# Optimization experiments

Hardware: AMD Instinct MI355X
Metric: run time of the kernel (lower is better)

The kernel has to match this reference:

```python
import jax, jax.numpy as jnp
import numpy as np
from jax import lax

B = 32768   # batch_size
M = 14      # letters per word
H, WD = 16, 8  # input_dim -> cout_numel = 128 (SAME padding, stride 1)
L = 26      # num_labels
KS = 5      # conv kernel size (conv_layers[0][-1])
F = H * WD


def setup_inputs() -> dict:
    key = jax.random.key(0)
    k1, k2, k3, k4, k5 = jax.random.split(key, 5)
    X = jax.random.normal(k1, (B, M, F), dtype=jnp.float32)
    K = jax.random.normal(k2, (1, 1, KS, KS), dtype=jnp.float32) * 0.1  # conv kernel (OIHW)
    b = jax.random.normal(k3, (1,), dtype=jnp.float32) * 0.1            # conv bias
    W = jax.random.normal(k4, (L, F), dtype=jnp.float32)                # emission weights
    T = jax.random.normal(k5, (L, L), dtype=jnp.float32)                # transition matrix
    return {"X": X, "K": K, "b": b, "W": W, "T": T}


def _conv_features(X, K, b):
    # each letter image is a (1,H,W) map; SAME conv keeps spatial dims -> F features
    words = X.reshape(B * M, 1, H, WD)
    out = lax.conv_general_dilated(
        words, K, window_strides=(1, 1), padding="SAME",
        dimension_numbers=("NCHW", "OIHW", "NCHW")) + b
    return out.reshape(B, M, F)


def _viterbi(score, T):
    # score: (M, L) emission scores for one word; Viterbi max-decode
    def step(v, s):  # v: (L,) best path value ending at each label
        tot = v[:, None] + T          # (prev L, next L)
        bp = jnp.argmax(tot, axis=0)  # best previous label per next label
        v_new = jnp.max(tot, axis=0) + s
        return v_new, bp

    v_last, bps = lax.scan(step, score[0], score[1:])  # bps: (M-1, L)
    last = jnp.argmax(v_last)

    def back(nxt, bp):
        cur = bp[nxt]
        return cur, cur

    _, idxs = lax.scan(back, last, bps, reverse=True)  # (M-1,)
    path = jnp.concatenate([idxs, last[None]])         # (M,)
    return path.astype(jnp.int32)


def reference(X, K, b, W, T):
    feats = _conv_features(X, K, b)                 # (B, M, F)
    scores = jnp.einsum("bmf,lf->bml", feats, W)    # (B, M, L) emission scores
    decods = jax.vmap(lambda s: _viterbi(s, T))(scores)  # (B, M)
    return decods[..., None]                        # (B, M, 1) int32, matches torch output
```

## Files before the change

### kernel.cpp

```cpp
#include <hip/hip_runtime.h>
#include <math.h>

#define LBL 26
#define MM  14
#define FF  128
#define HH  16
#define WW  8
#define KSZ 5
#define WPB 16
#define LPB (WPB * MM)
#define SST 29

__global__ void prep_kernel(const float* __restrict__ K,
                            const float* __restrict__ b,
                            const float* __restrict__ W,
                            float* __restrict__ w2,
                            float* __restrict__ cvec) {
    int idx = blockIdx.x * blockDim.x + threadIdx.x;
    int stride = gridDim.x * blockDim.x;
    for (int o = idx; o < LBL * FF; o += stride) {
        int l = o / FF, f = o % FF;
        int qy = f / WW, qx = f % WW;
        double acc = 0.0;
        for (int ky = 0; ky < KSZ; ++ky) {
            int y = qy - ky + 2;
            if (y < 0 || y >= HH) continue;
            for (int kx = 0; kx < KSZ; ++kx) {
                int x = qx - kx + 2;
                if (x < 0 || x >= WW) continue;
                acc += (double)K[ky * KSZ + kx] * (double)W[l * FF + y * WW + x];
            }
        }
        w2[o] = (float)acc;
    }
    for (int l = idx; l < LBL; l += stride) {
        double s = 0.0;
        for (int f = 0; f < FF; ++f) s += (double)W[l * FF + f];
        cvec[l] = (float)(s * (double)b[0]);
    }
}

__global__ __launch_bounds__(256) void fused_kernel(const float* __restrict__ X,
                                                    const float* __restrict__ w2,
                                                    const float* __restrict__ cvec,
                                                    const float* __restrict__ Tm,
                                                    int* __restrict__ out) {
    __shared__ float4 wtile[32][LBL];
    __shared__ float  s_lds[WPB][MM][SST];
    __shared__ float  vb[8][32];

    const int tid = threadIdx.x;
    const int blk = blockIdx.x;

    const float4* W4 = (const float4*)w2;
    for (int i = tid; i < 32 * LBL; i += 256) {
        const int l = i >> 5, q = i & 31;
        wtile[q][l] = W4[i];
    }
    __syncthreads();

    if (tid < LPB) {
        const int letter = blk * LPB + tid;
        const float4* xr = (const float4*)X + (size_t)letter * 32;

        float acc[LBL];
#pragma unroll
        for (int l = 0; l < LBL; ++l) acc[l] = cvec[l];

#define COMPUTE(g, C0, C1, C2, C3)                                         \
    {                                                                      \
        _Pragma("unroll")                                                  \
        for (int l = 0; l < LBL; ++l) {                                    \
            const float4 w0 = wtile[4 * (g) + 0][l];        \
            const float4 w1 = wtile[4 * (g) + 1][l];                       \
            const float4 w2v = wtile[4 * (g) + 2][l];                      \
            const float4 w3 = wtile[4 * (g) + 3][l];                       \
            float a = acc[l];                                              \
            a = fmaf(C0.x, w0.x, a); a = fmaf(C0.y, w0.y, a);              \
            a = fmaf(C0.z, w0.z, a); a = fmaf(C0.w, w0.w, a);              \
            a = fmaf(C1.x, w1.x, a); a = fmaf(C1.y, w1.y, a);              \
            a = fmaf(C1.z, w1.z, a); a = fmaf(C1.w, w1.w, a);              \
            a = fmaf(C2.x, w2v.x, a); a = fmaf(C2.y, w2v.y, a);            \
            a = fmaf(C2.z, w2v.z, a); a = fmaf(C2.w, w2v.w, a);            \
            a = fmaf(C3.x, w3.x, a); a = fmaf(C3.y, w3.y, a);              \
            a = fmaf(C3.z, w3.z, a); a = fmaf(C3.w, w3.w, a);              \
            acc[l] = a;                                                    \
        }                                                                  \
    }

        float4 c0 = xr[0], c1 = xr[1], c2 = xr[2], c3 = xr[3];
        for (int g = 0; g < 7; ++g) {
            const float4 n0 = xr[4 * g + 4], n1 = xr[4 * g + 5];
            const float4 n2 = xr[4 * g + 6], n3 = xr[4 * g + 7];
            COMPUTE(g, c0, c1, c2, c3)
            c0 = n0; c1 = n1; c2 = n2; c3 = n3;
        }
        COMPUTE(7, c0, c1, c2, c3)
#undef COMPUTE

        float* dst = &s_lds[0][0][0] + tid * SST;
#pragma unroll
        for (int l = 0; l < LBL; ++l) dst[l] = acc[l];
    }
    __syncthreads();

    const int wv   = tid >> 6;
    const int lane = tid & 63;
    const int half = lane >> 5;
    const int j    = lane & 31;
    const int jc   = (j < LBL) ? j : 25;

    const int wl = wv * 2 + half;

    float tcol[LBL];
#pragma unroll
    for (int i = 0; i < LBL; ++i) tcol[i] = Tm[i * LBL + jc];

    float* vbw = &vb[wl][0];

    for (int pass = 0; pass < 2; ++pass) {
        const int lwl  = pass * 8 + wl;
        const int word = blk * WPB + lwl;
        const float* sw = &s_lds[lwl][0][0];

        float v = (j < LBL) ? sw[j] : -INFINITY;
        vbw[j] = v;
        unsigned bp_pack[4] = {0u, 0u, 0u, 0u};

#pragma unroll
        for (int t = 1; t < MM; ++t) {
            const float se = sw[t * SST + jc];
            float best = -INFINITY;
            int bi = 0;
            const float4* q4 = (const float4*)vbw;
#define VCHK(vexpr, idx) { const float val = (vexpr) + tcol[idx]; \
                           if (val > best) { best = val; bi = idx; } }
            {
                float4 qq;
                qq = q4[0]; VCHK(qq.x, 0) VCHK(qq.y, 1) VCHK(qq.z, 2) VCHK(qq.w, 3)
                qq = q4[1]; VCHK(qq.x, 4) VCHK(qq.y, 5) VCHK(qq.z, 6) VCHK(qq.w, 7)
                qq = q4[2]; VCHK(qq.x, 8) VCHK(qq.y, 9) VCHK(qq.z, 10) VCHK(qq.w, 11)
                qq = q4[3]; VCHK(qq.x, 12) VCHK(qq.y, 13) VCHK(qq.z, 14) VCHK(qq.w, 15)
                qq = q4[4]; VCHK(qq.x, 16) VCHK(qq.y, 17) VCHK(qq.z, 18) VCHK(qq.w, 19)
                qq = q4[5]; VCHK(qq.x, 20) VCHK(qq.y, 21) VCHK(qq.z, 22) VCHK(qq.w, 23)
                qq = q4[6]; VCHK(qq.x, 24) VCHK(qq.y, 25)
            }
#undef VCHK
            v = (j < LBL) ? (best + se) : -INFINITY;
            vbw[j] = v;
            const int k = t - 1;
            bp_pack[k >> 2] |= (unsigned)bi << ((k & 3) * 8);
        }

        float best = v;
        int bidx = (j < LBL) ? j : 999;
#pragma unroll
        for (int d = 1; d < 32; d <<= 1) {
            const float ov = __shfl_xor(best, d, 64);
            const int oi = __shfl_xor(bidx, d, 64);
            if (ov > best || (ov == best && oi < bidx)) { best = ov; bidx = oi; }
        }

        int cur = bidx;
        if (j == 0) out[word * MM + (MM - 1)] = cur;
#pragma unroll
        for (int k = MM - 2; k >= 0; --k) {
            const unsigned packed = __shfl(bp_pack[k >> 2], (lane & 32) | cur, 64);
            cur = (int)((packed >> ((k & 3) * 8)) & 0xffu);
            if (j == 0) out[word * MM + k] = cur;
        }
    }
}

template <int PAD>
__global__ __launch_bounds__(256) void scores_kernel(const float* __restrict__ X,
                                                     const float* __restrict__ w2,
                                                     const float* __restrict__ cvec,
                                                     float* __restrict__ sV) {
    __shared__ float4 wtile[32][LBL];
    __shared__ float  slds[256 * LBL];

    const int tid    = threadIdx.x;
    const int letter = blockIdx.x * 256 + tid;

    const float4* W4 = (const float4*)w2;
    for (int i = tid; i < 32 * LBL; i += 256) {
        const int l = i >> 5, q = i & 31;
        wtile[q][l] = W4[i];
    }
    __syncthreads();

    const float4* xr = (const float4*)X + (size_t)letter * 32;

    float acc[LBL];
#pragma unroll
    for (int l = 0; l < LBL; ++l) acc[l] = cvec[l];

#define COMPUTE(g, C0, C1, C2, C3)                                         \
    {                                                                      \
        _Pragma("unroll")                                                  \
        for (int l = 0; l < LBL; ++l) {                                    \
            const float4 w0 = wtile[4 * (g) + 0][l];                       \
            const float4 w1 = wtile[4 * (g) + 1][l];                       \
            const float4 w2v = wtile[4 * (g) + 2][l];                      \
            const float4 w3 = wtile[4 * (g) + 3][l];                       \
            float a = acc[l];                                              \
            a = fmaf(C0.x, w0.x, a); a = fmaf(C0.y, w0.y, a);              \
            a = fmaf(C0.z, w0.z, a); a = fmaf(C0.w, w0.w, a);              \
            a = fmaf(C1.x, w1.x, a); a = fmaf(C1.y, w1.y, a);              \
            a = fmaf(C1.z, w1.z, a); a = fmaf(C1.w, w1.w, a);              \
            a = fmaf(C2.x, w2v.x, a); a = fmaf(C2.y, w2v.y, a);            \
            a = fmaf(C2.z, w2v.z, a); a = fmaf(C2.w, w2v.w, a);            \
            a = fmaf(C3.x, w3.x, a); a = fmaf(C3.y, w3.y, a);              \
            a = fmaf(C3.z, w3.z, a); a = fmaf(C3.w, w3.w, a);              \
            acc[l] = a;                                                    \
        }                                                                  \
    }

    float4 c0 = xr[0], c1 = xr[1], c2 = xr[2], c3 = xr[3];
    for (int g = 0; g < 7; ++g) {
        const float4 n0 = xr[4 * g + 4], n1 = xr[4 * g + 5];
        const float4 n2 = xr[4 * g + 6], n3 = xr[4 * g + 7];
        COMPUTE(g, c0, c1, c2, c3)
        c0 = n0; c1 = n1; c2 = n2; c3 = n3;
    }
    COMPUTE(7, c0, c1, c2, c3)
#undef COMPUTE

#pragma unroll
    for (int l = 0; l < LBL; ++l) slds[tid * LBL + l] = acc[l];
    __syncthreads();
    const size_t obase = (size_t)blockIdx.x * 256 * PAD;
    for (int idx = tid; idx < 256 * PAD; idx += 256) {
        const int ll = idx / PAD, lw = idx - ll * PAD;
        sV[obase + idx] = (lw < LBL) ? slds[ll * LBL + lw] : 0.0f;
    }
}

template <int PAD>
__global__ __launch_bounds__(256) void viterbi_kernel(const float* __restrict__ sV,
                                                      const float* __restrict__ Tm,
                                                      int* __restrict__ out) {
    __shared__ float T_lds[LBL * LBL];
    __shared__ float vb[8][32];

    const int tid  = threadIdx.x;
    for (int i = tid; i < LBL * LBL; i += 256) T_lds[i] = Tm[i];
    __syncthreads();

    const int wv   = tid >> 6;
    const int lane = tid & 63;
    const int half = lane >> 5;
    const int j    = lane & 31;
    const int jc   = (j < LBL) ? j : 25;

    const int wl   = wv * 2 + half;
    const int word = blockIdx.x * 8 + wl;
    const float* sw = sV + (size_t)word * (MM * PAD);

    float tcol[LBL];
#pragma unroll
    for (int i = 0; i < LBL; ++i) tcol[i] = T_lds[i * LBL + jc];

    float* vbw = &vb[wl][0];
    float v = (j < LBL) ? sw[j] : -INFINITY;
    vbw[j] = v;
    unsigned bp_pack[4] = {0u, 0u, 0u, 0u};

#pragma unroll
    for (int t = 1; t < MM; ++t) {
        const float se = sw[t * PAD + jc];
        float best = -INFINITY;
        int bi = 0;
        const float4* q4 = (const float4*)vbw;
#define VCHK(vexpr, idx) { const float val = (vexpr) + tcol[idx]; \
                           if (val > best) { best = val; bi = idx; } }
        {
            float4 qq;
            qq = q4[0]; VCHK(qq.x, 0) VCHK(qq.y, 1) VCHK(qq.z, 2) VCHK(qq.w, 3)
            qq = q4[1]; VCHK(qq.x, 4) VCHK(qq.y, 5) VCHK(qq.z, 6) VCHK(qq.w, 7)
            qq = q4[2]; VCHK(qq.x, 8) VCHK(qq.y, 9) VCHK(qq.z, 10) VCHK(qq.w, 11)
            qq = q4[3]; VCHK(qq.x, 12) VCHK(qq.y, 13) VCHK(qq.z, 14) VCHK(qq.w, 15)
            qq = q4[4]; VCHK(qq.x, 16) VCHK(qq.y, 17) VCHK(qq.z, 18) VCHK(qq.w, 19)
            qq = q4[5]; VCHK(qq.x, 20) VCHK(qq.y, 21) VCHK(qq.z, 22) VCHK(qq.w, 23)
            qq = q4[6]; VCHK(qq.x, 24) VCHK(qq.y, 25)
        }
#undef VCHK
        v = (j < LBL) ? (best + se) : -INFINITY;
        vbw[j] = v;
        const int k = t - 1;
        bp_pack[k >> 2] |= (unsigned)bi << ((k & 3) * 8);
    }

    float best = v;
    int bidx = (j < LBL) ? j : 999;
#pragma unroll
    for (int d = 1; d < 32; d <<= 1) {
        const float ov = __shfl_xor(best, d, 64);
        const int oi = __shfl_xor(bidx, d, 64);
        if (ov > best || (ov == best && oi < bidx)) { best = ov; bidx = oi; }
    }

    int cur = bidx;
    if (j == 0) out[word * MM + (MM - 1)] = cur;
#pragma unroll
    for (int k = MM - 2; k >= 0; --k) {
        const unsigned packed = __shfl(bp_pack[k >> 2], (lane & 32) | cur, 64);
        cur = (int)((packed >> ((k & 3) * 8)) & 0xffu);
        if (j == 0) out[word * MM + k] = cur;
    }
}

extern "C" void kernel_launch(void* const* d_in, const int* in_sizes, int n_in,
                              void* d_out, int out_size, void* d_ws, size_t ws_size,
                              hipStream_t stream) {
    const float* X = (const float*)d_in[0];
    const float* K = (const float*)d_in[1];
    const float* b = (const float*)d_in[2];
    const float* W = (const float*)d_in[3];
    const float* T = (const float*)d_in[4];
    int* out = (int*)d_out;

    const int nw = in_sizes[0] / (MM * FF);
    const int NLET = nw * MM;

    const size_t w_bytes = (size_t)(LBL * FF + LBL) * sizeof(float);
    const size_t sV28    = (size_t)NLET * 28 * sizeof(float);

    if ((NLET % LPB) == 0 && (nw % WPB) == 0 && ws_size >= w_bytes) {
        float* w2   = (float*)d_ws;
        float* cvec = w2 + LBL * FF;
        prep_kernel<<<(LBL * FF + 255) / 256, 256, 0, stream>>>(K, b, W, w2, cvec);
        fused_kernel<<<NLET / LPB, 256, 0, stream>>>(X, w2, cvec, T, out);
    } else if ((NLET % 256) == 0 && (nw % 8) == 0 && ws_size >= sV28 + w_bytes) {
        float* sV   = (float*)d_ws;
        float* w2   = (float*)((char*)d_ws + sV28);
        float* cvec = w2 + LBL * FF;
        prep_kernel<<<(LBL * FF + 255) / 256, 256, 0, stream>>>(K, b, W, w2, cvec);
        scores_kernel<28><<<NLET / 256, 256, 0, stream>>>(X, w2, cvec, sV);
        viterbi_kernel<28><<<nw / 8, 256, 0, stream>>>(sV, T, out);
    }
}
```

Before: 149.9 us.

## Fold conv-weight prep into scores kernel with packed FMA, drop fused kernel

Removes the fused single-kernel path and the separate prep kernel. The scores kernel now computes the conv-folded emission weights and bias vector in every block, in double precision, into an interleaved LDS layout. Its dot products use v_pk_fma_f32 over label pairs to halve FMA instruction count. The cost is redundant per-block weight preparation and a round trip of the score matrix through global memory into a separate Viterbi kernel, replacing the previous fused path.

```diff
diff --git a/kernel.cpp b/kernel.cpp
--- a/kernel.cpp
+++ b/kernel.cpp
@@ -7,9 +7,16 @@
 #define HH  16
 #define WW  8
 #define KSZ 5
-#define WPB 16
-#define LPB (WPB * MM)
-#define SST 29
+
+typedef float fv2 __attribute__((ext_vector_type(2)));
+
+__device__ __forceinline__ fv2 mkfv2(float a, float b) { fv2 r; r.x = a; r.y = b; return r; }
+
+__device__ __forceinline__ fv2 pkfma(fv2 a, fv2 b, fv2 c) {
+    fv2 d;
+    asm volatile("v_pk_fma_f32 %0, %1, %2, %3" : "=v"(d) : "v"(a), "v"(b), "v"(c));
+    return d;
+}
 
 __global__ void prep_kernel(const float* __restrict__ K,
                             const float* __restrict__ b,
@@ -40,143 +47,104 @@
     }
 }
 
-__global__ __launch_bounds__(256) void fused_kernel(const float* __restrict__ X,
-                                                    const float* __restrict__ w2,
-                                                    const float* __restrict__ cvec,
-                                                    const float* __restrict__ Tm,
-                                                    int* __restrict__ out) {
-    __shared__ float4 wtile[32][LBL];
-    __shared__ float  s_lds[WPB][MM][SST];
-    __shared__ float  vb[8][32];
-
-    const int tid = threadIdx.x;
-    const int blk = blockIdx.x;
-
-    const float4* W4 = (const float4*)w2;
-    for (int i = tid; i < 32 * LBL; i += 256) {
-        const int l = i >> 5, q = i & 31;
-        wtile[q][l] = W4[i];
-    }
-    __syncthreads();
-
-    if (tid < LPB) {
-        const int letter = blk * LPB + tid;
-        const float4* xr = (const float4*)X + (size_t)letter * 32;
-
-        float acc[LBL];
-#pragma unroll
-        for (int l = 0; l < LBL; ++l) acc[l] = cvec[l];
-
-#define COMPUTE(g, C0, C1, C2, C3)                                         \
-    {                                                                      \
-        _Pragma("unroll")                                                  \
-        for (int l = 0; l < LBL; ++l) {                                    \
-            const float4 w0 = wtile[4 * (g) + 0][l];        \
-            const float4 w1 = wtile[4 * (g) + 1][l];                       \
-            const float4 w2v = wtile[4 * (g) + 2][l];                      \
-            const float4 w3 = wtile[4 * (g) + 3][l];                       \
-            float a = acc[l];                                              \
-            a = fmaf(C0.x, w0.x, a); a = fmaf(C0.y, w0.y, a);              \
-            a = fmaf(C0.z, w0.z, a); a = fmaf(C0.w, w0.w, a);              \
-            a = fmaf(C1.x, w1.x, a); a = fmaf(C1.y, w1.y, a);              \
-            a = fmaf(C1.z, w1.z, a); a = fmaf(C1.w, w1.w, a);              \
-            a = fmaf(C2.x, w2v.x, a); a = fmaf(C2.y, w2v.y, a);            \
-            a = fmaf(C2.z, w2v.z, a); a = fmaf(C2.w, w2v.w, a);            \
-            a = fmaf(C3.x, w3.x, a); a = fmaf(C3.y, w3.y, a);              \
-            a = fmaf(C3.z, w3.z, a); a = fmaf(C3.w, w3.w, a);              \
-            acc[l] = a;                                                    \
-        }                                                                  \
-    }
-
-        float4 c0 = xr[0], c1 = xr[1], c2 = xr[2], c3 = xr[3];
-        for (int g = 0; g < 7; ++g) {
-            const float4 n0 = xr[4 * g + 4], n1 = xr[4 * g + 5];
-            const float4 n2 = xr[4 * g + 6], n3 = xr[4 * g + 7];
-            COMPUTE(g, c0, c1, c2, c3)
-            c0 = n0; c1 = n1; c2 = n2; c3 = n3;
-        }
-        COMPUTE(7, c0, c1, c2, c3)
-#undef COMPUTE
-
-        float* dst = &s_lds[0][0][0] + tid * SST;
-#pragma unroll
-        for (int l = 0; l < LBL; ++l) dst[l] = acc[l];
-    }
-    __syncthreads();
-
-    const int wv   = tid >> 6;
-    const int lane = tid & 63;
-    const int half = lane >> 5;
-    const int j    = lane & 31;
-    const int jc   = (j < LBL) ? j : 25;
-
-    const int wl = wv * 2 + half;
-
-    float tcol[LBL];
-#pragma unroll
-    for (int i = 0; i < LBL; ++i) tcol[i] = Tm[i * LBL + jc];
-
-    float* vbw = &vb[wl][0];
-
-    for (int pass = 0; pass < 2; ++pass) {
-        const int lwl  = pass * 8 + wl;
-        const int word = blk * WPB + lwl;
-        const float* sw = &s_lds[lwl][0][0];
-
-        float v = (j < LBL) ? sw[j] : -INFINITY;
-        vbw[j] = v;
-        unsigned bp_pack[4] = {0u, 0u, 0u, 0u};
-
-#pragma unroll
-        for (int t = 1; t < MM; ++t) {
-            const float se = sw[t * SST + jc];
-            float best = -INFINITY;
-            int bi = 0;
-            const float4* q4 = (const float4*)vbw;
-#define VCHK(vexpr, idx) { const float val = (vexpr) + tcol[idx]; \
-                           if (val > best) { best = val; bi = idx; } }
-            {
-                float4 qq;
-                qq = q4[0]; VCHK(qq.x, 0) VCHK(qq.y, 1) VCHK(qq.z, 2) VCHK(qq.w, 3)
-                qq = q4[1]; VCHK(qq.x, 4) VCHK(qq.y, 5) VCHK(qq.z, 6) VCHK(qq.w, 7)
-                qq = q4[2]; VCHK(qq.x, 8) VCHK(qq.y, 9) VCHK(qq.z, 10) VCHK(qq.w, 11)
-                qq = q4[3]; VCHK(qq.x, 12) VCHK(qq.y, 13) VCHK(qq.z, 14) VCHK(qq.w, 15)
-                qq = q4[4]; VCHK(qq.x, 16) VCHK(qq.y, 17) VCHK(qq.z, 18) VCHK(qq.w, 19)
-                qq = q4[5]; VCHK(qq.x, 20) VCHK(qq.y, 21) VCHK(qq.z, 22) VCHK(qq.w, 23)
-                qq = q4[6]; VCHK(qq.x, 24) VCHK(qq.y, 25)
-            }
-#undef VCHK
-            v = (j < LBL) ? (best + se) : -INFINITY;
-            vbw[j] = v;
-            const int k = t - 1;
-            bp_pack[k >> 2] |= (unsigned)bi << ((k & 3) * 8);
-        }
-
-        float best = v;
-        int bidx = (j < LBL) ? j : 999;
-#pragma unroll
-        for (int d = 1; d < 32; d <<= 1) {
-            const float ov = __shfl_xor(best, d, 64);
-            const int oi = __shfl_xor(bidx, d, 64);
-            if (ov > best || (ov == best && oi < bidx)) { best = ov; bidx = oi; }
-        }
-
-        int cur = bidx;
-        if (j == 0) out[word * MM + (MM - 1)] = cur;
-#pragma unroll
-        for (int k = MM - 2; k >= 0; --k) {
-            const unsigned packed = __shfl(bp_pack[k >> 2], (lane & 32) | cur, 64);
-            cur = (int)((packed >> ((k & 3) * 8)) & 0xffu);
-            if (j == 0) out[word * MM + k] = cur;
-        }
-    }
-}
-
 template <int PAD>
 __global__ __launch_bounds__(256) void scores_kernel(const float* __restrict__ X,
-                                                     const float* __restrict__ w2,
-                                                     const float* __restrict__ cvec,
+                                                     const float* __restrict__ K,
+                                                     const float* __restrict__ bb,
+                                                     const float* __restrict__ W,
                                                      float* __restrict__ sV) {
+    __shared__ float4 wt4[64][13];
+    __shared__ float  cv[32];
+    __shared__ float  slds[256 * LBL];
+
+    const int tid    = threadIdx.x;
+    const int letter = blockIdx.x * 256 + tid;
+
+    for (int o = tid; o < LBL * FF; o += 256) {
+        const int l = o / FF, f = o % FF;
+        const int qy = f / WW, qx = f % WW;
+        double acc = 0.0;
+        for (int ky = 0; ky < KSZ; ++ky) {
+            const int y = qy - ky + 2;
+            if (y < 0 || y >= HH) continue;
+            for (int kx = 0; kx < KSZ; ++kx) {
+                const int x = qx - kx + 2;
+                if (x < 0 || x >= WW) continue;
+                acc += (double)K[ky * KSZ + kx] * (double)W[l * FF + y * WW + x];
+            }
+        }
+        ((float*)&wt4[f >> 1][l >> 1])[(f & 1) * 2 + (l & 1)] = (float)acc;
+    }
+    if (tid < LBL) {
+        double s = 0.0;
+        for (int f = 0; f < FF; ++f) s += (double)W[tid * FF + f];
+        cv[tid] = (float)(s * (double)bb[0]);
+    }
+    __syncthreads();
+
+    const float4* xr = (const float4*)X + (size_t)letter * 32;
+
+    fv2 acc2[13];
+#pragma unroll
+    for (int lp = 0; lp < 13; ++lp) acc2[lp] = mkfv2(cv[2 * lp], cv[2 * lp + 1]);
+
+#define FMA2(xs, w01, a) pkfma(mkfv2((xs), (xs)), (w01), (a))
+
+#define COMPUTE(g, C0, C1, C2, C3)                                               \
+    {                                                                            \
+        _Pragma("unroll")                                                        \
+        for (int lp = 0; lp < 13; ++lp) {                                        \
+            fv2 a = acc2[lp];                                                    \
+            float4 t; fv2 wlo, whi;                                              \
+            t = wt4[8 * (g) + 0][lp]; wlo = *(fv2*)&t.x; whi = *(fv2*)&t.z;      \
+            a = FMA2(C0.x, wlo, a); a = FMA2(C0.y, whi, a);                      \
+            t = wt4[8 * (g) + 1][lp]; wlo = *(fv2*)&t.x; whi = *(fv2*)&t.z;      \
+            a = FMA2(C0.z, wlo, a); a = FMA2(C0.w, whi, a);                      \
+            t = wt4[8 * (g) + 2][lp]; wlo = *(fv2*)&t.x; whi = *(fv2*)&t.z;      \
+            a = FMA2(C1.x, wlo, a); a = FMA2(C1.y, whi, a);                      \
+            t = wt4[8 * (g) + 3][lp]; wlo = *(fv2*)&t.x; whi = *(fv2*)&t.z;      \
+            a = FMA2(C1.z, wlo, a); a = FMA2(C1.w, whi, a);                      \
+            t = wt4[8 * (g) + 4][lp]; wlo = *(fv2*)&t.x; whi = *(fv2*)&t.z;      \
+            a = FMA2(C2.x, wlo, a); a = FMA2(C2.y, whi, a);                      \
+            t = wt4[8 * (g) + 5][lp]; wlo = *(fv2*)&t.x; whi = *(fv2*)&t.z;      \
+            a = FMA2(C2.z, wlo, a); a = FMA2(C2.w, whi, a);                      \
+            t = wt4[8 * (g) + 6][lp]; wlo = *(fv2*)&t.x; whi = *(fv2*)&t.z;      \
+            a = FMA2(C3.x, wlo, a); a = FMA2(C3.y, whi, a);                      \
+            t = wt4[8 * (g) + 7][lp]; wlo = *(fv2*)&t.x; whi = *(fv2*)&t.z;      \
+            a = FMA2(C3.z, wlo, a); a = FMA2(C3.w, whi, a);                      \
+            acc2[lp] = a;                                                        \
+        }                                                                        \
+    }
+
+    float4 c0 = xr[0], c1 = xr[1], c2 = xr[2], c3 = xr[3];
+    for (int g = 0; g < 7; ++g) {
+        const float4 n0 = xr[4 * g + 4], n1 = xr[4 * g + 5];
+        const float4 n2 = xr[4 * g + 6], n3 = xr[4 * g + 7];
+        COMPUTE(g, c0, c1, c2, c3)
+        c0 = n0; c1 = n1; c2 = n2; c3 = n3;
+    }
+    COMPUTE(7, c0, c1, c2, c3)
+#undef COMPUTE
+#undef FMA2
+
+#pragma unroll
+    for (int lp = 0; lp < 13; ++lp) {
+        slds[tid * LBL + 2 * lp]     = acc2[lp].x;
+        slds[tid * LBL + 2 * lp + 1] = acc2[lp].y;
+    }
+    __syncthreads();
+    const size_t obase = (size_t)blockIdx.x * 256 * PAD;
+    for (int idx = tid; idx < 256 * PAD; idx += 256) {
+        const int ll = idx / PAD, lw = idx - ll * PAD;
+        sV[obase + idx] = (lw < LBL) ? slds[ll * LBL + lw] : 0.0f;
+    }
+}
+
+template <int PAD>
+__global__ __launch_bounds__(256) void scores_kernel_fb(const float* __restrict__ X,
+                                                        const float* __restrict__ w2,
+                                                        const float* __restrict__ cvec,
+                                                        float* __restrict__ sV) {
     __shared__ float4 wtile[32][LBL];
     __shared__ float  slds[256 * LBL];
 
@@ -326,18 +294,20 @@
 
     const size_t w_bytes = (size_t)(LBL * FF + LBL) * sizeof(float);
     const size_t sV28    = (size_t)NLET * 28 * sizeof(float);
-
-    if ((NLET % LPB) == 0 && (nw % WPB) == 0 && ws_size >= w_bytes) {
-        float* w2   = (float*)d_ws;
+    const size_t sV26    = (size_t)NLET * 26 * sizeof(float);
+
+    const bool shape_ok = (NLET % 256) == 0 && (nw % 8) == 0;
+
+    if (shape_ok && ws_size >= sV28) {
+        float* sV = (float*)d_ws;
+        scores_kernel<28><<<NLET / 256, 256, 0, stream>>>(X, K, b, W, sV);
+        viterbi_kernel<28><<<nw / 8, 256, 0, stream>>>(sV, T, out);
+    } else if (shape_ok && ws_size >= sV26 + w_bytes) {
+        float* sV   = (float*)d_ws;
+        float* w2   = (float*)((char*)d_ws + sV26);
         float* cvec = w2 + LBL * FF;
         prep_kernel<<<(LBL * FF + 255) / 256, 256, 0, stream>>>(K, b, W, w2, cvec);
-        fused_kernel<<<NLET / LPB, 256, 0, stream>>>(X, w2, cvec, T, out);
-    } else if ((NLET % 256) == 0 && (nw % 8) == 0 && ws_size >= sV28 + w_bytes) {
-        float* sV   = (float*)d_ws;
-        float* w2   = (float*)((char*)d_ws + sV28);
-        float* cvec = w2 + LBL * FF;
-        prep_kernel<<<(LBL * FF + 255) / 256, 256, 0, stream>>>(K, b, W, w2, cvec);
-        scores_kernel<28><<<NLET / 256, 256, 0, stream>>>(X, w2, cvec, sV);
-        viterbi_kernel<28><<<nw / 8, 256, 0, stream>>>(sV, T, out);
-    }
-}
+        scores_kernel_fb<26><<<NLET / 256, 256, 0, stream>>>(X, w2, cvec, sV);
+        viterbi_kernel<26><<<nw / 8, 256, 0, stream>>>(sV, T, out);
+    }
+}
```

Measured after the change: 198.9 us. 1.33x slower.
